# Optimization experiments

Hardware: AMD Instinct MI355X
Metric: run time of the kernel (lower is better)

The kernel has to match this reference:

```python
import jax, jax.numpy as jnp
import numpy as np

PI = float(np.pi)


def _layernorm(x, g, b, eps=1e-5):
    mu = jnp.mean(x, axis=-1, keepdims=True)
    var = jnp.var(x, axis=-1, keepdims=True)
    return (x - mu) * jax.lax.rsqrt(var + eps) * g + b


def setup_inputs() -> dict:
    key = jax.random.key(0)
    B, L, D, P = 4, 2048, 256, 32
    ks = jax.random.split(key, 16)

    def lin_w(k, fi, fo):
        return (jax.random.normal(k, (fi, fo), dtype=jnp.float32) / np.sqrt(fi)).astype(jnp.float32)

    inp = {
        'x': jax.random.normal(ks[0], (B, L, D), dtype=jnp.float32),
        'pos_phases': jax.random.normal(ks[1], (L, P), dtype=jnp.float32) * PI,
        'w_mem1v': lin_w(ks[2], D, P), 'b_mem1v': jnp.zeros((P,), jnp.float32),
        'w_mem1o': lin_w(ks[3], P, D), 'b_mem1o': jnp.zeros((D,), jnp.float32),
        'w_off': lin_w(ks[4], D + P, P), 'b_off': jnp.zeros((P,), jnp.float32),
        'w_key': lin_w(ks[5], D, P), 'b_key': jnp.zeros((P,), jnp.float32),
        'w_val': lin_w(ks[6], D, D), 'b_val': jnp.zeros((D,), jnp.float32),
        'w_sk1': lin_w(ks[7], 2 * D, D), 'b_sk1': jnp.zeros((D,), jnp.float32),
        'w_sk2': lin_w(ks[8], D, P), 'b_sk2': jnp.zeros((P,), jnp.float32),
        'w_gate': lin_w(ks[9], D, 1), 'b_gate': jnp.zeros((1,), jnp.float32),
        'ln_g': jnp.ones((D,), jnp.float32), 'ln_b': jnp.zeros((D,), jnp.float32),
        'w_out': lin_w(ks[10], D, D), 'b_out': jnp.zeros((D,), jnp.float32),
    }
    return inp


def reference(x, pos_phases, w_mem1v, b_mem1v, w_mem1o, b_mem1o, w_off, b_off,
              w_key, b_key, w_val, b_val, w_sk1, b_sk1, w_sk2, b_sk2,
              w_gate, b_gate, ln_g, ln_b, w_out, b_out):
    B, L, D = x.shape
    P = pos_phases.shape[-1]

    pos_cos = jnp.cos(pos_phases)  # [L,P]
    pos_sin = jnp.sin(pos_phases)

    # Memory 1: flat [B,L,P] phasor cumulative memory
    v1 = x @ w_mem1v + b_mem1v                       # [B,L,P]
    mem1_cos = jnp.cumsum(pos_cos[None] * v1, axis=1)
    mem1_sin = jnp.cumsum(pos_sin[None] * v1, axis=1)

    offset_input = jnp.concatenate([x, jnp.broadcast_to(pos_phases[None], (B, L, P))], axis=-1)
    offset = jnp.tanh(offset_input @ w_off + b_off) * PI
    oc, os = jnp.cos(offset), jnp.sin(offset)
    query_cos = pos_cos[None] * oc - pos_sin[None] * os
    query_sin = pos_sin[None] * oc + pos_cos[None] * os
    pos_ret = (mem1_cos * query_cos + mem1_sin * query_sin) / np.sqrt(P)
    pos_out = pos_ret @ w_mem1o + b_mem1o            # [B,L,D]

    # Memory 2: full [B,L,P,D] phasor KV cumulative memory
    key_phases = jnp.tanh(x @ w_key + b_key) * PI    # [B,L,P]
    key_cos, key_sin = jnp.cos(key_phases), jnp.sin(key_phases)
    values = x @ w_val + b_val                       # [B,L,D]
    store_gate = jax.nn.sigmoid(x @ w_gate + b_gate) # [B,L,1]

    positions = jnp.arange(1, L + 1, dtype=x.dtype)[None, :, None]
    context_avg = jnp.cumsum(x, axis=1) / positions
    h = jax.nn.gelu(jnp.concatenate([x, context_avg], axis=-1) @ w_sk1 + b_sk1, approximate=False)
    storage_phases = jnp.tanh(h @ w_sk2 + b_sk2) * PI  # [B,L,P]

    gated_v = values * store_gate                    # [B,L,D]
    kv_mem_cos = jnp.cumsum(jnp.cos(storage_phases)[..., None] * gated_v[:, :, None, :], axis=1)  # [B,L,P,D]
    kv_mem_sin = jnp.cumsum(jnp.sin(storage_phases)[..., None] * gated_v[:, :, None, :], axis=1)

    gate_cumsum = jnp.clip(jnp.cumsum(store_gate, axis=1), 1.0, None)  # [B,L,1]
    kv_retrieved = jnp.einsum('blpd,blp->bld', kv_mem_cos, key_cos) + \
                   jnp.einsum('blpd,blp->bld', kv_mem_sin, key_sin)
    kv_retrieved = kv_retrieved / (jnp.sqrt(gate_cumsum) * np.sqrt(P))

    combined = pos_out + kv_retrieved
    return x + _layernorm(combined, ln_g, ln_b) @ w_out + b_out
```

## Files before the change

### kernel.cpp

```cpp
#include <hip/hip_runtime.h>
#include <hip/hip_bf16.h>

constexpr int B_ = 4;
constexpr int L_ = 2048;
constexpr int D_ = 256;
constexpr int P_ = 32;
constexpr int CL = 32;
constexpr int NC = L_ / CL;

#define PI_F 3.14159265358979323846f
#define INV_SQRT_P 0.17677669529663687f

typedef __attribute__((ext_vector_type(8))) short short8_t;
typedef __attribute__((ext_vector_type(4))) float floatx4;

static __device__ inline short f2bf(float f) {
  unsigned int u;
  __builtin_memcpy(&u, &f, 4);
  unsigned int r = (u + 0x7fffu + ((u >> 16) & 1u)) >> 16;
  return (short)r;
}
static __device__ inline float bf2f(short s) {
  unsigned int u = ((unsigned int)(unsigned short)s) << 16;
  float f;
  __builtin_memcpy(&f, &u, 4);
  return f;
}

__global__ void wprep(const float* __restrict__ x, const float* __restrict__ pos,
                      const float* __restrict__ w_val, const float* __restrict__ w_mem1v,
                      const float* __restrict__ w_off, const float* __restrict__ b_off,
                      const float* __restrict__ w_key, const float* __restrict__ w_gate,
                      const float* __restrict__ w_sk1, const float* __restrict__ w_out,
                      const float* __restrict__ w_sk2, const float* __restrict__ w_mem1o,
                      short* __restrict__ WA, short* __restrict__ W1,
                      short* __restrict__ WO, short* __restrict__ W2T,
                      short* __restrict__ W1OT,
                      short* __restrict__ xbf, float* __restrict__ poff,
                      float* __restrict__ ctxsum) {
  int blk = blockIdx.x, tid = threadIdx.x;
  if (blk < 384) {
    int idx = blk * 256 + tid;
    int n = idx >> 8, k = idx & 255;
    float v;
    if (n < 256) v = w_val[k * 256 + n];
    else if (n < 288) v = w_mem1v[k * 32 + (n - 256)];
    else if (n < 320) v = w_off[k * 32 + (n - 288)];
    else if (n < 352) v = w_key[k * 32 + (n - 320)];
    else if (n == 352) v = w_gate[k];
    else v = 0.f;
    WA[idx] = f2bf(v);
  } else if (blk < 896) {
    int idx = (blk - 384) * 256 + tid;
    int n = idx >> 9, k = idx & 511;
    W1[idx] = f2bf(w_sk1[k * 256 + n]);
  } else if (blk < 1152) {
    int idx = (blk - 896) * 256 + tid;
    int n = idx >> 8, k = idx & 255;
    WO[idx] = f2bf(w_out[k * 256 + n]);
  } else if (blk < 1184) {
    int idx = (blk - 1152) * 256 + tid;
    int p = idx >> 8, k = idx & 255;
    W2T[idx] = f2bf(w_sk2[k * 32 + p]);
  } else if (blk < 1216) {
    int idx = (blk - 1184) * 256 + tid;
    int d = idx >> 5, p = idx & 31;
    W1OT[idx] = f2bf(w_mem1o[p * 256 + d]);
  } else if (blk < 3264) {
    int idx = ((blk - 1216) * 256 + tid) * 4;
    float4 v = *(const float4*)&x[idx];
    short4 o;
    o.x = f2bf(v.x); o.y = f2bf(v.y); o.z = f2bf(v.z); o.w = f2bf(v.w);
    *(short4*)&xbf[idx] = o;
  } else if (blk < 3520) {
    int idx = (blk - 3264) * 256 + tid;
    int l = idx >> 5, p = idx & 31;
    float a = b_off[p];
    for (int j = 0; j < 32; ++j) a += pos[l * 32 + j] * w_off[(256 + j) * 32 + p];
    poff[idx] = a;
  } else {
    int c2 = blk - 3520;
    int b = c2 >> 6, ch = c2 & 63;
    int xb = (b * L_ + ch * 32) * 256 + tid;
    float s = 0.f;
#pragma unroll 8
    for (int i = 0; i < 32; ++i) s += x[xb + i * 256];
    ctxsum[c2 * 256 + tid] = s;
  }
}

template <int KTILES, int NBLK, int MODE>
__global__ __launch_bounds__(256) void gemm_k(const short* __restrict__ A0,
                                              const short* __restrict__ A1,
                                              const short* __restrict__ W,
                                              const float* __restrict__ bias,
                                              const float* __restrict__ xres,
                                              float* __restrict__ outf,
                                              short* __restrict__ outb) {
  __shared__ short As[64][136];
  __shared__ short Bs[64][136];
  int tid = threadIdx.x;
  int mg = blockIdx.x / NBLK, ng = blockIdx.x % NBLK;
  int tok0 = mg * 64, n0 = ng * 64;
  int lane = tid & 63, w = tid >> 6;
  int mw = (w & 1) * 32, nw = (w >> 1) * 32;
  floatx4 acc[2][2] = {{{0.f, 0.f, 0.f, 0.f}, {0.f, 0.f, 0.f, 0.f}},
                       {{0.f, 0.f, 0.f, 0.f}, {0.f, 0.f, 0.f, 0.f}}};
  int r2 = tid >> 4, c8 = tid & 15;
  int ml = lane & 15, kq = (lane >> 4) * 8;
  const int K = KTILES * 128;

  for (int kt = 0; kt < KTILES; ++kt) {
    const short* Asrc;
    int cb;
    if (KTILES == 4) {
      Asrc = (kt < 2) ? A0 : A1;
      cb = (kt & 1) * 128;
    } else {
      Asrc = A0;
      cb = kt * 128;
    }
#pragma unroll
    for (int pass = 0; pass < 4; ++pass) {
      int row = pass * 16 + r2;
      *(short8_t*)&As[row][c8 * 8] =
          *(const short8_t*)&Asrc[(tok0 + row) * 256 + cb + c8 * 8];
      *(short8_t*)&Bs[row][c8 * 8] =
          *(const short8_t*)&W[(n0 + row) * K + kt * 128 + c8 * 8];
    }
    __syncthreads();
#pragma unroll
    for (int s = 0; s < 4; ++s) {
      short8_t a0 = *(short8_t*)&As[mw + ml][s * 32 + kq];
      short8_t a1 = *(short8_t*)&As[mw + 16 + ml][s * 32 + kq];
      short8_t b0 = *(short8_t*)&Bs[nw + ml][s * 32 + kq];
      short8_t b1 = *(short8_t*)&Bs[nw + 16 + ml][s * 32 + kq];
      acc[0][0] = __builtin_amdgcn_mfma_f32_16x16x32_bf16(a0, b0, acc[0][0], 0, 0, 0);
      acc[0][1] = __builtin_amdgcn_mfma_f32_16x16x32_bf16(a0, b1, acc[0][1], 0, 0, 0);
      acc[1][0] = __builtin_amdgcn_mfma_f32_16x16x32_bf16(a1, b0, acc[1][0], 0, 0, 0);
      acc[1][1] = __builtin_amdgcn_mfma_f32_16x16x32_bf16(a1, b1, acc[1][1], 0, 0, 0);
    }
    __syncthreads();
  }
  int col = lane & 15, rq = (lane >> 4) * 4;
#pragma unroll
  for (int nt = 0; nt < 2; ++nt) {
    int n = n0 + nw + nt * 16 + col;
    float bv = (MODE == 0) ? 0.f : bias[n];
#pragma unroll
    for (int mt = 0; mt < 2; ++mt) {
#pragma unroll
      for (int rg = 0; rg < 4; ++rg) {
        int tok = tok0 + mw + mt * 16 + rq + rg;
        float v = acc[mt][nt][rg] + bv;
        if (MODE == 0) {
          outb[tok * 384 + n] = f2bf(v);
        } else if (MODE == 1) {
          float g = 0.5f * v * (1.f + erff(v * 0.70710678118654752f));
          outb[tok * 256 + n] = f2bf(g);
        } else {
          outf[tok * 256 + n] = xres[tok * 256 + n] + v;
        }
      }
    }
  }
}

__global__ __launch_bounds__(384) void gemmA3(const short* __restrict__ xbf,
                                              const short* __restrict__ WA,
                                              const float* __restrict__ pos,
                                              const float* __restrict__ poff,
                                              const float* __restrict__ b_mem1v,
                                              const float* __restrict__ b_key,
                                              const float* __restrict__ b_gate,
                                              const float* __restrict__ b_val,
                                              float* __restrict__ m1cT,
                                              float* __restrict__ m1sT,
                                              float* __restrict__ qc,
                                              float* __restrict__ qs,
                                              short* __restrict__ K2bf,
                                              short* __restrict__ gvT,
                                              float* __restrict__ sg) {
  __shared__ float YL[32][132];
  __shared__ float gsh[32];
  int tid = threadIdx.x;
  int lane = tid & 63, w = tid >> 6;
  int ml = lane & 15, quad = lane >> 4, kq = quad * 8;
  int bc = blockIdx.x;
  int tok0 = bc * 32;
  floatx4 acc[2][4] = {};
  const short* A0p = &xbf[(tok0 + ml) * 256 + kq];
  const short* A1p = &xbf[(tok0 + 16 + ml) * 256 + kq];
  const short* Bp = &WA[(w * 64 + ml) * 256 + kq];
#pragma unroll
  for (int ks = 0; ks < 8; ++ks) {
    short8_t a0 = *(const short8_t*)(A0p + ks * 32);
    short8_t a1 = *(const short8_t*)(A1p + ks * 32);
#pragma unroll
    for (int nt = 0; nt < 4; ++nt) {
      short8_t b = *(const short8_t*)(Bp + nt * 16 * 256 + ks * 32);
      acc[0][nt] = __builtin_amdgcn_mfma_f32_16x16x32_bf16(a0, b, acc[0][nt], 0, 0, 0);
      acc[1][nt] = __builtin_amdgcn_mfma_f32_16x16x32_bf16(a1, b, acc[1][nt], 0, 0, 0);
    }
  }
  if (w >= 4) {
#pragma unroll
    for (int mt = 0; mt < 2; ++mt)
#pragma unroll
      for (int nt = 0; nt < 4; ++nt) {
        int col = (w - 4) * 64 + nt * 16 + ml;
#pragma unroll
        for (int r = 0; r < 4; ++r)
          YL[mt * 16 + quad * 4 + r][col] = acc[mt][nt][r];
      }
  }
  __syncthreads();
  if (tid < 256) {
#pragma unroll
    for (int it = 0; it < 4; ++it) {
      int idx = it * 256 + tid;
      int t = idx >> 5, p = idx & 31;
      int tok = tok0 + t, l = tok & (L_ - 1);
      int b = tok >> 11;
      float v1 = YL[t][p] + b_mem1v[p];
      float ph = pos[l * 32 + p];
      float pc = cosf(ph), ps = sinf(ph);
      int idxT = (b * 32 + p) * L_ + l;
      m1cT[idxT] = pc * v1;
      m1sT[idxT] = ps * v1;
      float off = tanhf(YL[t][32 + p] + poff[l * 32 + p]) * PI_F;
      float oc = cosf(off), os = sinf(off);
      int gidx = tok * 32 + p;
      qc[gidx] = pc * oc - ps * os;
      qs[gidx] = ps * oc + pc * os;
      float kp = tanhf(YL[t][64 + p] + b_key[p]) * PI_F;
      K2bf[tok * 64 + p] = f2bf(cosf(kp));
      K2bf[tok * 64 + 32 + p] = f2bf(sinf(kp));
      if (p == 0) {
        float g = 1.f / (1.f + expf(-(YL[t][96] + b_gate[0])));
        sg[tok] = g;
        gsh[t] = g;
      }
    }
  }
  __syncthreads();
  if (w < 4) {
#pragma unroll
    for (int nt = 0; nt < 4; ++nt) {
      int d = w * 64 + nt * 16 + ml;
      float bv = b_val[d];
#pragma unroll
      for (int mt = 0; mt < 2; ++mt) {
        int t0 = mt * 16 + quad * 4;
        short4 o;
        o.x = f2bf((acc[mt][nt][0] + bv) * gsh[t0 + 0]);
        o.y = f2bf((acc[mt][nt][1] + bv) * gsh[t0 + 1]);
        o.z = f2bf((acc[mt][nt][2] + bv) * gsh[t0 + 2]);
        o.w = f2bf((acc[mt][nt][3] + bv) * gsh[t0 + 3]);
        *(short4*)&gvT[(bc * 256 + d) * 32 + t0] = o;
      }
    }
  }
}

__global__ void scan_all(float* __restrict__ m1cT, float* __restrict__ m1sT,
                         float* __restrict__ sg, const float* __restrict__ x,
                         const float* __restrict__ ctxsum, short* __restrict__ ctxbf) {
  int blk = blockIdx.x;
  int tid = threadIdx.x;
  if (blk >= 260) {
    int c2 = blk - 260;
    int b = c2 >> 6, ch = c2 & 63;
    float run = 0.f;
    int sb = b * 64 * 256 + tid;
    for (int c = 0; c < ch; ++c) run += ctxsum[sb + c * 256];
    int xb = (b * L_ + ch * 32) * 256 + tid;
#pragma unroll 8
    for (int i = 0; i < 32; ++i) {
      run += x[xb + i * 256];
      int l = ch * 32 + i;
      ctxbf[xb + i * 256] = f2bf(run / (float)(l + 1));
    }
    return;
  }
  int lane = tid & 63, wid = tid >> 6;
  __shared__ float wsum[4];
  float carry = 0.f;
  float* arr;
  int base;
  if (blk < 256) {
    arr = (blk < 128) ? m1cT : m1sT;
    base = (blk & 127) * L_;
  } else {
    arr = sg;
    base = (blk - 256) * L_;
  }
  for (int t0 = 0; t0 < L_; t0 += 256) {
    int l = t0 + tid;
    float v = arr[base + l];
#pragma unroll
    for (int off = 1; off < 64; off <<= 1) {
      float n = __shfl_up(v, off, 64);
      if (lane >= off) v += n;
    }
    if (lane == 63) wsum[wid] = v;
    __syncthreads();
    float add = carry;
    for (int w = 0; w < wid; ++w) add += wsum[w];
    arr[base + l] = v + add;
    carry += wsum[0] + wsum[1] + wsum[2] + wsum[3];
    __syncthreads();
  }
}

__global__ __launch_bounds__(256) void kernelCD(const short* __restrict__ hs,
                                                const short* __restrict__ W2T,
                                                const float* __restrict__ b_sk2,
                                                const short* __restrict__ gvT,
                                                short* __restrict__ SPbf,
                                                short* __restrict__ UT) {
  __shared__ __align__(16) short SPL[2][64][40];
  int tid = threadIdx.x;
  int tok0 = blockIdx.x * 64;
  int lane = tid & 63, w = tid >> 6;
  int ml = lane & 15, quad = lane >> 4, kq = quad * 8;
  int m0 = w * 16;
  floatx4 pacc[2] = {};
#pragma unroll
  for (int s = 0; s < 8; ++s) {
    short8_t a = *(const short8_t*)&hs[(tok0 + m0 + ml) * 256 + s * 32 + kq];
    short8_t b0 = *(const short8_t*)&W2T[ml * 256 + s * 32 + kq];
    short8_t b1 = *(const short8_t*)&W2T[(16 + ml) * 256 + s * 32 + kq];
    pacc[0] = __builtin_amdgcn_mfma_f32_16x16x32_bf16(a, b0, pacc[0], 0, 0, 0);
    pacc[1] = __builtin_amdgcn_mfma_f32_16x16x32_bf16(a, b1, pacc[1], 0, 0, 0);
  }
  int cl = w >> 1;
#pragma unroll
  for (int nt = 0; nt < 2; ++nt) {
    int p = nt * 16 + ml;
    float bs = b_sk2[p];
#pragma unroll
    for (int r = 0; r < 4; ++r) {
      int tok = tok0 + m0 + quad * 4 + r;
      float sp = tanhf(pacc[nt][r] + bs) * PI_F;
      short c = f2bf(cosf(sp)), s = f2bf(sinf(sp));
      int tl = (w & 1) * 16 + quad * 4 + r;
      SPL[cl][p][tl] = c;
      SPL[cl][32 + p][tl] = s;
      SPbf[tok * 64 + p] = c;
      SPbf[tok * 64 + 32 + p] = s;
    }
  }
  __syncthreads();
  int c2 = w & 1, dbase = (w >> 1) * 128;
  int bc = blockIdx.x * 2 + c2;
  short8_t a[4];
#pragma unroll
  for (int mt = 0; mt < 4; ++mt) a[mt] = *(short8_t*)&SPL[c2][mt * 16 + ml][kq];
#pragma unroll
  for (int dp = 0; dp < 2; ++dp) {
    floatx4 acc[4][4] = {};
#pragma unroll
    for (int nt = 0; nt < 4; ++nt) {
      short8_t b = *(const short8_t*)&gvT[(bc * 256 + dbase + dp * 64 + nt * 16 + ml) * 32 + kq];
#pragma unroll
      for (int mt = 0; mt < 4; ++mt)
        acc[mt][nt] = __builtin_amdgcn_mfma_f32_16x16x32_bf16(a[mt], b, acc[mt][nt], 0, 0, 0);
    }
#pragma unroll
    for (int mt = 0; mt < 4; ++mt)
#pragma unroll
      for (int nt = 0; nt < 4; ++nt)
#pragma unroll
        for (int r = 0; r < 4; ++r) {
          int q = mt * 16 + quad * 4 + r;
          int d = dbase + dp * 64 + nt * 16 + ml;
          UT[(bc * 256 + d) * 64 + q] = f2bf(acc[mt][nt][r]);
        }
  }
}

__global__ void kernelE(short* __restrict__ UT) {
  int tid = blockIdx.x * 256 + threadIdx.x;
  int q = tid & 63;
  int d = (tid >> 6) & 255;
  int b = tid >> 14;
  int base = ((b * NC) * 256 + d) * 64 + q;
  const int cs = 256 * 64;
  float run = 0.f;
  for (int c0 = 0; c0 < NC; c0 += 8) {
    short v[8];
#pragma unroll
    for (int j = 0; j < 8; ++j) v[j] = UT[base + (c0 + j) * cs];
#pragma unroll
    for (int j = 0; j < 8; ++j) {
      UT[base + (c0 + j) * cs] = f2bf(run);
      run += bf2f(v[j]);
    }
  }
}

__global__ __launch_bounds__(256) void kernelFG(const short* __restrict__ UT,
                                                const short* __restrict__ SPbf,
                                                const short* __restrict__ K2bf,
                                                const short* __restrict__ gvT,
                                                const float* __restrict__ sgc,
                                                const float* __restrict__ m1cT,
                                                const float* __restrict__ m1sT,
                                                const float* __restrict__ qc,
                                                const float* __restrict__ qs,
                                                const short* __restrict__ W1OT,
                                                const float* __restrict__ b_mem1o,
                                                const float* __restrict__ ln_g,
                                                const float* __restrict__ ln_b,
                                                short* __restrict__ cbn) {
  __shared__ __align__(16) short SL[32][40];
  __shared__ __align__(16) short PR[32][40];
  __shared__ float CMB[32][260];
  __shared__ float scl[32], mu_s[32], rs_s[32];
  int tid = threadIdx.x;
  int bc = blockIdx.x;
  int lbase = bc * CL;
  int bb = bc >> 6, lloc = (bc & 63) * 32;
  if (tid < 32) scl[tid] = rsqrtf(fmaxf(sgc[lbase + tid], 1.f)) * INV_SQRT_P;
  for (int it = 0; it < 4; ++it) {
    int i = it * 256 + tid;
    int p = i >> 5, t = i & 31;
    int gT = (bb * 32 + p) * L_ + lloc + t;
    int g = (lbase + t) * 32 + p;
    PR[t][p] = f2bf((m1cT[gT] * qc[g] + m1sT[gT] * qs[g]) * INV_SQRT_P);
  }
  int lane = tid & 63, w = tid >> 6;
  int ml = lane & 15, quad = lane >> 4, kq = quad * 8;
  floatx4 acc[2][4] = {};
  short8_t ka0 = *(const short8_t*)&K2bf[(lbase + ml) * 64 + kq];
  short8_t ka1 = *(const short8_t*)&K2bf[(lbase + 16 + ml) * 64 + kq];
  short8_t kb0 = *(const short8_t*)&K2bf[(lbase + ml) * 64 + 32 + kq];
  short8_t kb1 = *(const short8_t*)&K2bf[(lbase + 16 + ml) * 64 + 32 + kq];
#pragma unroll
  for (int nt = 0; nt < 4; ++nt) {
    short8_t b = *(const short8_t*)&UT[(bc * 256 + w * 64 + nt * 16 + ml) * 64 + kq];
    acc[0][nt] = __builtin_amdgcn_mfma_f32_16x16x32_bf16(ka0, b, acc[0][nt], 0, 0, 0);
    acc[1][nt] = __builtin_amdgcn_mfma_f32_16x16x32_bf16(ka1, b, acc[1][nt], 0, 0, 0);
  }
  if (w == 0) {
    floatx4 sacc[2][2] = {};
#pragma unroll
    for (int ks2 = 0; ks2 < 2; ++ks2) {
      short8_t a0 = (ks2 == 0) ? ka0 : kb0;
      short8_t a1 = (ks2 == 0) ? ka1 : kb1;
      short8_t b0 = *(const short8_t*)&SPbf[(lbase + ml) * 64 + ks2 * 32 + kq];
      short8_t b1 = *(const short8_t*)&SPbf[(lbase + 16 + ml) * 64 + ks2 * 32 + kq];
      sacc[0][0] = __builtin_amdgcn_mfma_f32_16x16x32_bf16(a0, b0, sacc[0][0], 0, 0, 0);
      sacc[0][1] = __builtin_amdgcn_mfma_f32_16x16x32_bf16(a0, b1, sacc[0][1], 0, 0, 0);
      sacc[1][0] = __builtin_amdgcn_mfma_f32_16x16x32_bf16(a1, b0, sacc[1][0], 0, 0, 0);
      sacc[1][1] = __builtin_amdgcn_mfma_f32_16x16x32_bf16(a1, b1, sacc[1][1], 0, 0, 0);
    }
#pragma unroll
    for (int mt = 0; mt < 2; ++mt)
#pragma unroll
      for (int nt = 0; nt < 2; ++nt)
#pragma unroll
        for (int r = 0; r < 4; ++r) {
          int trow = mt * 16 + quad * 4 + r;
          int scol = nt * 16 + ml;
          float v = (scol <= trow) ? sacc[mt][nt][r] : 0.f;
          SL[trow][scol] = f2bf(v);
        }
  }
  __syncthreads();
#pragma unroll
  for (int nt = 0; nt < 4; ++nt) {
    short8_t b = *(const short8_t*)&UT[(bc * 256 + w * 64 + nt * 16 + ml) * 64 + 32 + kq];
    acc[0][nt] = __builtin_amdgcn_mfma_f32_16x16x32_bf16(kb0, b, acc[0][nt], 0, 0, 0);
    acc[1][nt] = __builtin_amdgcn_mfma_f32_16x16x32_bf16(kb1, b, acc[1][nt], 0, 0, 0);
  }
  {
    short8_t a0 = *(short8_t*)&SL[ml][kq];
    short8_t a1 = *(short8_t*)&SL[16 + ml][kq];
#pragma unroll
    for (int nt = 0; nt < 4; ++nt) {
      short8_t b = *(const short8_t*)&gvT[(bc * 256 + w * 64 + nt * 16 + ml) * 32 + kq];
      acc[0][nt] = __builtin_amdgcn_mfma_f32_16x16x32_bf16(a0, b, acc[0][nt], 0, 0, 0);
      acc[1][nt] = __builtin_amdgcn_mfma_f32_16x16x32_bf16(a1, b, acc[1][nt], 0, 0, 0);
    }
  }
  floatx4 macc[2][4] = {};
  {
    short8_t a0 = *(short8_t*)&PR[ml][kq];
    short8_t a1 = *(short8_t*)&PR[16 + ml][kq];
#pragma unroll
    for (int nt = 0; nt < 4; ++nt) {
      short8_t b = *(const short8_t*)&W1OT[(w * 64 + nt * 16 + ml) * 32 + kq];
      macc[0][nt] = __builtin_amdgcn_mfma_f32_16x16x32_bf16(a0, b, macc[0][nt], 0, 0, 0);
      macc[1][nt] = __builtin_amdgcn_mfma_f32_16x16x32_bf16(a1, b, macc[1][nt], 0, 0, 0);
    }
  }
#pragma unroll
  for (int mt = 0; mt < 2; ++mt)
#pragma unroll
    for (int nt = 0; nt < 4; ++nt) {
      int d = w * 64 + nt * 16 + ml;
      float bm = b_mem1o[d];
#pragma unroll
      for (int r = 0; r < 4; ++r) {
        int t = mt * 16 + quad * 4 + r;
        CMB[t][d] = acc[mt][nt][r] * scl[t] + macc[mt][nt][r] + bm;
      }
    }
  __syncthreads();
  {
    int t = tid >> 3, g = tid & 7;
    float s = 0.f, s2 = 0.f;
#pragma unroll
    for (int j = 0; j < 32; ++j) {
      float v = CMB[t][g + j * 8];
      s += v;
      s2 += v * v;
    }
#pragma unroll
    for (int m = 1; m < 8; m <<= 1) {
      s += __shfl_xor(s, m, 64);
      s2 += __shfl_xor(s2, m, 64);
    }
    if (g == 0) {
      float mu = s / (float)D_;
      float var = s2 / (float)D_ - mu * mu;
      mu_s[t] = mu;
      rs_s[t] = rsqrtf(var + 1e-5f);
    }
  }
  __syncthreads();
  {
    float lg = ln_g[tid], lb = ln_b[tid];
#pragma unroll
    for (int t = 0; t < 32; ++t)
      cbn[(lbase + t) * 256 + tid] = f2bf((CMB[t][tid] - mu_s[t]) * rs_s[t] * lg + lb);
  }
}

extern "C" void kernel_launch(void* const* d_in, const int* in_sizes, int n_in,
                              void* d_out, int out_size, void* d_ws, size_t ws_size,
                              hipStream_t stream) {
  const float* x = (const float*)d_in[0];
  const float* pos = (const float*)d_in[1];
  const float* w_mem1v = (const float*)d_in[2];
  const float* b_mem1v = (const float*)d_in[3];
  const float* w_mem1o = (const float*)d_in[4];
  const float* b_mem1o = (const float*)d_in[5];
  const float* w_off = (const float*)d_in[6];
  const float* b_off = (const float*)d_in[7];
  const float* w_key = (const float*)d_in[8];
  const float* b_key = (const float*)d_in[9];
  const float* w_val = (const float*)d_in[10];
  const float* b_val = (const float*)d_in[11];
  const float* w_sk1 = (const float*)d_in[12];
  const float* b_sk1 = (const float*)d_in[13];
  const float* w_sk2 = (const float*)d_in[14];
  const float* b_sk2 = (const float*)d_in[15];
  const float* w_gate = (const float*)d_in[16];
  const float* b_gate = (const float*)d_in[17];
  const float* ln_g = (const float*)d_in[18];
  const float* ln_b = (const float*)d_in[19];
  const float* w_out = (const float*)d_in[20];
  const float* b_out = (const float*)d_in[21];
  float* out = (float*)d_out;
  float* ws = (float*)d_ws;

  const int BLP = B_ * L_ * P_;
  const int BLD = B_ * L_ * D_;
  float* m1cT = ws;
  float* m1sT = m1cT + BLP;
  float* qc = m1sT + BLP;
  float* qs = qc + BLP;
  float* sg = qs + BLP;
  float* poff = sg + B_ * L_;
  float* ctxsum = poff + L_ * P_;
  short* UT = (short*)(ctxsum + B_ * 64 * 256);
  short* xbf = UT + (size_t)B_ * NC * 256 * 64;
  short* cbn = xbf;
  short* ctxbf = xbf + BLD;
  short* hs = ctxbf + BLD;
  short* gvT = hs + BLD;
  short* K2bf = gvT + BLD;
  short* SPbf = K2bf + B_ * L_ * 64;
  short* WA = SPbf + B_ * L_ * 64;
  short* W1 = WA + 384 * 256;
  short* WO = W1 + 256 * 512;
  short* W2T = WO + 256 * 256;
  short* W1OT = W2T + 32 * 256;

  wprep<<<3776, 256, 0, stream>>>(x, pos, w_val, w_mem1v, w_off, b_off, w_key, w_gate,
                                  w_sk1, w_out, w_sk2, w_mem1o, WA, W1, WO, W2T, W1OT,
                                  xbf, poff, ctxsum);
  gemmA3<<<256, 384, 0, stream>>>(xbf, WA, pos, poff, b_mem1v, b_key, b_gate, b_val,
                                  m1cT, m1sT, qc, qs, K2bf, gvT, sg);
  scan_all<<<516, 256, 0, stream>>>(m1cT, m1sT, sg, x, ctxsum, ctxbf);
  gemm_k<4, 4, 1><<<128 * 4, 256, 0, stream>>>(xbf, ctxbf, W1, b_sk1, nullptr, nullptr, hs);
  kernelCD<<<(B_ * L_) / 64, 256, 0, stream>>>(hs, W2T, b_sk2, gvT, SPbf, UT);
  kernelE<<<256, 256, 0, stream>>>(UT);
  kernelFG<<<B_ * NC, 256, 0, stream>>>(UT, SPbf, K2bf, gvT, sg, m1cT, m1sT, qc, qs,
                                        W1OT, b_mem1o, ln_g, ln_b, cbn);
  gemm_k<2, 4, 2><<<128 * 4, 256, 0, stream>>>(cbn, nullptr, WO, b_out, x, out, nullptr);
}
```

Baseline: 186.9 us.

## Rebalance work splits in CD, FG and scan kernels for more parallelism

kernelCD now processes one 32-token chunk per block with twice as many blocks, and each wave computes a 16x16 slice of the projection. kernelFG uses 512 threads per block, so each wave covers 32 output columns, and the layernorm reduction and store are adjusted to match. kernelE and scan_all now issue all their global loads up front, so more loads are in flight before the serial accumulation starts. The aim is higher occupancy and better latency hiding, at the cost of more registers per thread (64 shorts in kernelE) and more blocks.

```diff
diff --git a/kernel.cpp b/kernel.cpp
--- a/kernel.cpp
+++ b/kernel.cpp
@@ -295,19 +295,22 @@
     arr = sg;
     base = (blk - 256) * L_;
   }
-  for (int t0 = 0; t0 < L_; t0 += 256) {
-    int l = t0 + tid;
-    float v = arr[base + l];
+  float v[8];
+#pragma unroll
+  for (int i = 0; i < 8; ++i) v[i] = arr[base + i * 256 + tid];
+#pragma unroll
+  for (int i = 0; i < 8; ++i) {
+    float vv = v[i];
 #pragma unroll
     for (int off = 1; off < 64; off <<= 1) {
-      float n = __shfl_up(v, off, 64);
-      if (lane >= off) v += n;
-    }
-    if (lane == 63) wsum[wid] = v;
+      float n = __shfl_up(vv, off, 64);
+      if (lane >= off) vv += n;
+    }
+    if (lane == 63) wsum[wid] = vv;
     __syncthreads();
     float add = carry;
     for (int w = 0; w < wid; ++w) add += wsum[w];
-    arr[base + l] = v + add;
+    arr[base + i * 256 + tid] = vv + add;
     carry += wsum[0] + wsum[1] + wsum[2] + wsum[3];
     __syncthreads();
   }
@@ -319,65 +322,57 @@
                                                 const short* __restrict__ gvT,
                                                 short* __restrict__ SPbf,
                                                 short* __restrict__ UT) {
-  __shared__ __align__(16) short SPL[2][64][40];
+  __shared__ __align__(16) short SPL[64][40];
   int tid = threadIdx.x;
-  int tok0 = blockIdx.x * 64;
+  int bc = blockIdx.x;
+  int tok0 = bc * 32;
   int lane = tid & 63, w = tid >> 6;
   int ml = lane & 15, quad = lane >> 4, kq = quad * 8;
-  int m0 = w * 16;
-  floatx4 pacc[2] = {};
+  int th = w & 1, ph = w >> 1;
+  floatx4 pacc = {};
 #pragma unroll
   for (int s = 0; s < 8; ++s) {
-    short8_t a = *(const short8_t*)&hs[(tok0 + m0 + ml) * 256 + s * 32 + kq];
-    short8_t b0 = *(const short8_t*)&W2T[ml * 256 + s * 32 + kq];
-    short8_t b1 = *(const short8_t*)&W2T[(16 + ml) * 256 + s * 32 + kq];
-    pacc[0] = __builtin_amdgcn_mfma_f32_16x16x32_bf16(a, b0, pacc[0], 0, 0, 0);
-    pacc[1] = __builtin_amdgcn_mfma_f32_16x16x32_bf16(a, b1, pacc[1], 0, 0, 0);
-  }
-  int cl = w >> 1;
-#pragma unroll
-  for (int nt = 0; nt < 2; ++nt) {
-    int p = nt * 16 + ml;
+    short8_t a = *(const short8_t*)&hs[(tok0 + th * 16 + ml) * 256 + s * 32 + kq];
+    short8_t b0 = *(const short8_t*)&W2T[(ph * 16 + ml) * 256 + s * 32 + kq];
+    pacc = __builtin_amdgcn_mfma_f32_16x16x32_bf16(a, b0, pacc, 0, 0, 0);
+  }
+  {
+    int p = ph * 16 + ml;
     float bs = b_sk2[p];
 #pragma unroll
     for (int r = 0; r < 4; ++r) {
-      int tok = tok0 + m0 + quad * 4 + r;
-      float sp = tanhf(pacc[nt][r] + bs) * PI_F;
+      int tl = th * 16 + quad * 4 + r;
+      int tok = tok0 + tl;
+      float sp = tanhf(pacc[r] + bs) * PI_F;
       short c = f2bf(cosf(sp)), s = f2bf(sinf(sp));
-      int tl = (w & 1) * 16 + quad * 4 + r;
-      SPL[cl][p][tl] = c;
-      SPL[cl][32 + p][tl] = s;
+      SPL[p][tl] = c;
+      SPL[32 + p][tl] = s;
       SPbf[tok * 64 + p] = c;
       SPbf[tok * 64 + 32 + p] = s;
     }
   }
   __syncthreads();
-  int c2 = w & 1, dbase = (w >> 1) * 128;
-  int bc = blockIdx.x * 2 + c2;
   short8_t a[4];
 #pragma unroll
-  for (int mt = 0; mt < 4; ++mt) a[mt] = *(short8_t*)&SPL[c2][mt * 16 + ml][kq];
-#pragma unroll
-  for (int dp = 0; dp < 2; ++dp) {
-    floatx4 acc[4][4] = {};
-#pragma unroll
-    for (int nt = 0; nt < 4; ++nt) {
-      short8_t b = *(const short8_t*)&gvT[(bc * 256 + dbase + dp * 64 + nt * 16 + ml) * 32 + kq];
-#pragma unroll
-      for (int mt = 0; mt < 4; ++mt)
-        acc[mt][nt] = __builtin_amdgcn_mfma_f32_16x16x32_bf16(a[mt], b, acc[mt][nt], 0, 0, 0);
-    }
+  for (int mt = 0; mt < 4; ++mt) a[mt] = *(short8_t*)&SPL[mt * 16 + ml][kq];
+  floatx4 acc[4][4] = {};
+#pragma unroll
+  for (int nt = 0; nt < 4; ++nt) {
+    short8_t b = *(const short8_t*)&gvT[(bc * 256 + w * 64 + nt * 16 + ml) * 32 + kq];
 #pragma unroll
     for (int mt = 0; mt < 4; ++mt)
-#pragma unroll
-      for (int nt = 0; nt < 4; ++nt)
-#pragma unroll
-        for (int r = 0; r < 4; ++r) {
-          int q = mt * 16 + quad * 4 + r;
-          int d = dbase + dp * 64 + nt * 16 + ml;
-          UT[(bc * 256 + d) * 64 + q] = f2bf(acc[mt][nt][r]);
-        }
-  }
+      acc[mt][nt] = __builtin_amdgcn_mfma_f32_16x16x32_bf16(a[mt], b, acc[mt][nt], 0, 0, 0);
+  }
+#pragma unroll
+  for (int mt = 0; mt < 4; ++mt)
+#pragma unroll
+    for (int nt = 0; nt < 4; ++nt)
+#pragma unroll
+      for (int r = 0; r < 4; ++r) {
+        int q = mt * 16 + quad * 4 + r;
+        int d = w * 64 + nt * 16 + ml;
+        UT[(bc * 256 + d) * 64 + q] = f2bf(acc[mt][nt][r]);
+      }
 }
 
 __global__ void kernelE(short* __restrict__ UT) {
@@ -387,20 +382,18 @@
   int b = tid >> 14;
   int base = ((b * NC) * 256 + d) * 64 + q;
   const int cs = 256 * 64;
+  short v[64];
+#pragma unroll
+  for (int c = 0; c < 64; ++c) v[c] = UT[base + c * cs];
   float run = 0.f;
-  for (int c0 = 0; c0 < NC; c0 += 8) {
-    short v[8];
-#pragma unroll
-    for (int j = 0; j < 8; ++j) v[j] = UT[base + (c0 + j) * cs];
-#pragma unroll
-    for (int j = 0; j < 8; ++j) {
-      UT[base + (c0 + j) * cs] = f2bf(run);
-      run += bf2f(v[j]);
-    }
-  }
-}
-
-__global__ __launch_bounds__(256) void kernelFG(const short* __restrict__ UT,
+#pragma unroll
+  for (int c = 0; c < 64; ++c) {
+    UT[base + c * cs] = f2bf(run);
+    run += bf2f(v[c]);
+  }
+}
+
+__global__ __launch_bounds__(512) void kernelFG(const short* __restrict__ UT,
                                                 const short* __restrict__ SPbf,
                                                 const short* __restrict__ K2bf,
                                                 const short* __restrict__ gvT,
@@ -423,8 +416,9 @@
   int lbase = bc * CL;
   int bb = bc >> 6, lloc = (bc & 63) * 32;
   if (tid < 32) scl[tid] = rsqrtf(fmaxf(sgc[lbase + tid], 1.f)) * INV_SQRT_P;
-  for (int it = 0; it < 4; ++it) {
-    int i = it * 256 + tid;
+#pragma unroll
+  for (int it = 0; it < 2; ++it) {
+    int i = it * 512 + tid;
     int p = i >> 5, t = i & 31;
     int gT = (bb * 32 + p) * L_ + lloc + t;
     int g = (lbase + t) * 32 + p;
@@ -432,14 +426,15 @@
   }
   int lane = tid & 63, w = tid >> 6;
   int ml = lane & 15, quad = lane >> 4, kq = quad * 8;
-  floatx4 acc[2][4] = {};
+  int d0 = w * 32;
+  floatx4 acc[2][2] = {};
   short8_t ka0 = *(const short8_t*)&K2bf[(lbase + ml) * 64 + kq];
   short8_t ka1 = *(const short8_t*)&K2bf[(lbase + 16 + ml) * 64 + kq];
   short8_t kb0 = *(const short8_t*)&K2bf[(lbase + ml) * 64 + 32 + kq];
   short8_t kb1 = *(const short8_t*)&K2bf[(lbase + 16 + ml) * 64 + 32 + kq];
 #pragma unroll
-  for (int nt = 0; nt < 4; ++nt) {
-    short8_t b = *(const short8_t*)&UT[(bc * 256 + w * 64 + nt * 16 + ml) * 64 + kq];
+  for (int nt = 0; nt < 2; ++nt) {
+    short8_t b = *(const short8_t*)&UT[(bc * 256 + d0 + nt * 16 + ml) * 64 + kq];
     acc[0][nt] = __builtin_amdgcn_mfma_f32_16x16x32_bf16(ka0, b, acc[0][nt], 0, 0, 0);
     acc[1][nt] = __builtin_amdgcn_mfma_f32_16x16x32_bf16(ka1, b, acc[1][nt], 0, 0, 0);
   }
@@ -470,8 +465,8 @@
   }
   __syncthreads();
 #pragma unroll
-  for (int nt = 0; nt < 4; ++nt) {
-    short8_t b = *(const short8_t*)&UT[(bc * 256 + w * 64 + nt * 16 + ml) * 64 + 32 + kq];
+  for (int nt = 0; nt < 2; ++nt) {
+    short8_t b = *(const short8_t*)&UT[(bc * 256 + d0 + nt * 16 + ml) * 64 + 32 + kq];
     acc[0][nt] = __builtin_amdgcn_mfma_f32_16x16x32_bf16(kb0, b, acc[0][nt], 0, 0, 0);
     acc[1][nt] = __builtin_amdgcn_mfma_f32_16x16x32_bf16(kb1, b, acc[1][nt], 0, 0, 0);
   }
@@ -479,19 +474,19 @@
     short8_t a0 = *(short8_t*)&SL[ml][kq];
     short8_t a1 = *(short8_t*)&SL[16 + ml][kq];
 #pragma unroll
-    for (int nt = 0; nt < 4; ++nt) {
-      short8_t b = *(const short8_t*)&gvT[(bc * 256 + w * 64 + nt * 16 + ml) * 32 + kq];
+    for (int nt = 0; nt < 2; ++nt) {
+      short8_t b = *(const short8_t*)&gvT[(bc * 256 + d0 + nt * 16 + ml) * 32 + kq];
       acc[0][nt] = __builtin_amdgcn_mfma_f32_16x16x32_bf16(a0, b, acc[0][nt], 0, 0, 0);
       acc[1][nt] = __builtin_amdgcn_mfma_f32_16x16x32_bf16(a1, b, acc[1][nt], 0, 0, 0);
     }
   }
-  floatx4 macc[2][4] = {};
+  floatx4 macc[2][2] = {};
   {
     short8_t a0 = *(short8_t*)&PR[ml][kq];
     short8_t a1 = *(short8_t*)&PR[16 + ml][kq];
 #pragma unroll
-    for (int nt = 0; nt < 4; ++nt) {
-      short8_t b = *(const short8_t*)&W1OT[(w * 64 + nt * 16 + ml) * 32 + kq];
+    for (int nt = 0; nt < 2; ++nt) {
+      short8_t b = *(const short8_t*)&W1OT[(d0 + nt * 16 + ml) * 32 + kq];
       macc[0][nt] = __builtin_amdgcn_mfma_f32_16x16x32_bf16(a0, b, macc[0][nt], 0, 0, 0);
       macc[1][nt] = __builtin_amdgcn_mfma_f32_16x16x32_bf16(a1, b, macc[1][nt], 0, 0, 0);
     }
@@ -499,8 +494,8 @@
 #pragma unroll
   for (int mt = 0; mt < 2; ++mt)
 #pragma unroll
-    for (int nt = 0; nt < 4; ++nt) {
-      int d = w * 64 + nt * 16 + ml;
+    for (int nt = 0; nt < 2; ++nt) {
+      int d = d0 + nt * 16 + ml;
       float bm = b_mem1o[d];
 #pragma unroll
       for (int r = 0; r < 4; ++r) {
@@ -510,16 +505,16 @@
     }
   __syncthreads();
   {
-    int t = tid >> 3, g = tid & 7;
+    int t = tid >> 4, g = tid & 15;
     float s = 0.f, s2 = 0.f;
 #pragma unroll
-    for (int j = 0; j < 32; ++j) {
-      float v = CMB[t][g + j * 8];
+    for (int j = 0; j < 16; ++j) {
+      float v = CMB[t][g + j * 16];
       s += v;
       s2 += v * v;
     }
 #pragma unroll
-    for (int m = 1; m < 8; m <<= 1) {
+    for (int m = 1; m < 16; m <<= 1) {
       s += __shfl_xor(s, m, 64);
       s2 += __shfl_xor(s2, m, 64);
     }
@@ -532,10 +527,13 @@
   }
   __syncthreads();
   {
-    float lg = ln_g[tid], lb = ln_b[tid];
-#pragma unroll
-    for (int t = 0; t < 32; ++t)
-      cbn[(lbase + t) * 256 + tid] = f2bf((CMB[t][tid] - mu_s[t]) * rs_s[t] * lg + lb);
+    int d = tid & 255, th = tid >> 8;
+    float lg = ln_g[d], lb = ln_b[d];
+#pragma unroll
+    for (int i = 0; i < 16; ++i) {
+      int t = th * 16 + i;
+      cbn[(lbase + t) * 256 + d] = f2bf((CMB[t][d] - mu_s[t]) * rs_s[t] * lg + lb);
+    }
   }
 }
 
@@ -597,9 +595,9 @@
                                   m1cT, m1sT, qc, qs, K2bf, gvT, sg);
   scan_all<<<516, 256, 0, stream>>>(m1cT, m1sT, sg, x, ctxsum, ctxbf);
   gemm_k<4, 4, 1><<<128 * 4, 256, 0, stream>>>(xbf, ctxbf, W1, b_sk1, nullptr, nullptr, hs);
-  kernelCD<<<(B_ * L_) / 64, 256, 0, stream>>>(hs, W2T, b_sk2, gvT, SPbf, UT);
+  kernelCD<<<(B_ * L_) / 32, 256, 0, stream>>>(hs, W2T, b_sk2, gvT, SPbf, UT);
   kernelE<<<256, 256, 0, stream>>>(UT);
-  kernelFG<<<B_ * NC, 256, 0, stream>>>(UT, SPbf, K2bf, gvT, sg, m1cT, m1sT, qc, qs,
+  kernelFG<<<B_ * NC, 512, 0, stream>>>(UT, SPbf, K2bf, gvT, sg, m1cT, m1sT, qc, qs,
                                         W1OT, b_mem1o, ln_g, ln_b, cbn);
   gemm_k<2, 4, 2><<<128 * 4, 256, 0, stream>>>(cbn, nullptr, WO, b_out, x, out, nullptr);
 }
```

Measured after the change: 180.3 us. -3.5%, faster.
